# Kernel tuning notes

Measured on AMD Instinct MI355X. Metric: run time of the kernel, lower is better.

The kernel has to match this reference:

```python
import jax, jax.numpy as jnp
import numpy as np

N_NODES = 100000
N_EDGES = 1600000
IN_CH = 128
OUT_CH = 128
N_REL = 8


def setup_inputs() -> dict:
    key = jax.random.key(0)
    k1, k2, k3, k4, k5, k6 = jax.random.split(key, 6)
    x = jax.random.normal(k1, (N_NODES, IN_CH), dtype=jnp.float32)
    edge_index = jax.random.randint(k2, (2, N_EDGES), 0, N_NODES, dtype=jnp.int64)
    edge_type = jax.random.randint(k3, (N_EDGES,), 0, N_REL, dtype=jnp.int64)
    # learned parameters (PyG RGCNConv: per-relation weight, root weight, bias)
    scale = 1.0 / np.sqrt(IN_CH)
    weight = jax.random.normal(k4, (N_REL, IN_CH, OUT_CH), dtype=jnp.float32) * scale
    root = jax.random.normal(k5, (IN_CH, OUT_CH), dtype=jnp.float32) * scale
    bias = jax.random.normal(k6, (OUT_CH,), dtype=jnp.float32) * 0.01
    return {"x": x, "edge_index": edge_index, "edge_type": edge_type,
            "weight": weight, "root": root, "bias": bias}


def reference(x, edge_index, edge_type, weight, root, bias):
    # PyG RGCNConv forward: out_i = x_i @ root + bias
    #   + sum_r mean_{j in N_r(i)} (x_j @ W_r)   (default aggr='mean' per relation)
    N = x.shape[0]
    R, _, O = weight.shape
    src, dst = edge_index[0], edge_index[1]
    # transform all nodes under every relation once: [R, N, O]
    xW = jnp.einsum('ni,rio->rno', x, weight)
    msg = xW[edge_type, src]                      # [E, O] per-edge message
    seg = edge_type * N + dst                     # segment per (relation, dst)
    sums = jax.ops.segment_sum(msg, seg, num_segments=R * N)        # [R*N, O]
    cnt = jax.ops.segment_sum(jnp.ones_like(msg[:, 0]), seg, num_segments=R * N)
    mean = sums / jnp.maximum(cnt, 1.0)[:, None]
    agg = mean.reshape(R, N, O).sum(axis=0)       # sum over relations
    return agg + x @ root + bias
```

## Files before the change

kernel.cpp:

```cpp
#include <hip/hip_runtime.h>
#include <hip/hip_bf16.h>
#include <stdint.h>

#define N_NODES 100000
#define N_EDGES 1600000
#define CH 128
#define N_REL 8
#define N_PAD 100096
#define N_KEYS (N_NODES * N_REL)

#define NBKT 782
#define NSUB 64
#define SUBCAP 128
#define BKT_STRIDE (NSUB * SUBCAP)
#define CUR_PAD 16
#define N_KEYS_PAD (NBKT * 1024)

using frag_ab = __attribute__((ext_vector_type(8))) short;
using frag_cd = __attribute__((ext_vector_type(4))) float;

__device__ __forceinline__ short f2bs(float f) {
    union { __hip_bfloat16 h; short s; } u;
    u.h = __float2bfloat16(f);
    return u.s;
}

__device__ __forceinline__ uint32_t pack2bf(float a, float b) {
    union { __hip_bfloat16 h; unsigned short s; } ua, ub;
    ua.h = __float2bfloat16(a); ub.h = __float2bfloat16(b);
    return (uint32_t)ua.s | ((uint32_t)ub.s << 16);
}

__device__ __forceinline__ float bf_lo(uint32_t u) { return __uint_as_float(u << 16); }
__device__ __forceinline__ float bf_hi(uint32_t u) { return __uint_as_float(u & 0xffff0000u); }


__global__ __launch_bounds__(256)
void prep_kernel(const int* __restrict__ ei, const int* __restrict__ et,
                 int* __restrict__ cur, uint32_t* __restrict__ bucket,
                 const float* __restrict__ x, short* __restrict__ xb,
                 const float* __restrict__ root, const float* __restrict__ W,
                 short* __restrict__ Bsw) {
    const int tid = threadIdx.x;
    const int g = blockIdx.x * 256 + tid;

    if (g < N_EDGES) {
        int dst = ei[N_EDGES + g];
        int src = ei[g];
        int r = et[g];
        int b = dst >> 7;
        int sub = blockIdx.x & (NSUB - 1);
        int pos = atomicAdd(&cur[(sub * NBKT + b) * CUR_PAD], 1);
        if (pos < SUBCAP)
            bucket[((size_t)b * NSUB + sub) * SUBCAP + pos] =
                ((uint32_t)src << 10) | ((uint32_t)(dst & 127) << 3) | (uint32_t)r;
    }

    if (g < N_NODES * CH / 8) {
        const float4* xp = (const float4*)x;
        float4 a = xp[(size_t)g * 2], bb = xp[(size_t)g * 2 + 1];
        frag_ab f;
        f[0] = f2bs(a.x); f[1] = f2bs(a.y); f[2] = f2bs(a.z); f[3] = f2bs(a.w);
        f[4] = f2bs(bb.x); f[5] = f2bs(bb.y); f[6] = f2bs(bb.z); f[7] = f2bs(bb.w);
        *(frag_ab*)(xb + (size_t)g * 8) = f;
    }

    if (g < 9 * 2048) {
        int chunk = g >> 11, entry = g & 2047;
        int m16 = entry & 15, ct = (entry >> 4) & 7, quad = (entry >> 7) & 3, ks = entry >> 9;
        const float* src = (chunk == 0) ? root : W + (size_t)(chunk - 1) * CH * CH;
        int col = ct * 16 + m16, kb = ks * 32 + quad * 8;
        frag_ab f;
#pragma unroll
        for (int j = 0; j < 8; ++j) f[j] = f2bs(src[(size_t)(kb + j) * CH + col]);
        *(frag_ab*)(Bsw + (size_t)g * 8) = f;
    }
}

__global__ __launch_bounds__(512)
void bin_kernel(const int* __restrict__ cur, const uint32_t* __restrict__ bucket,
                int* __restrict__ perm, int* __restrict__ ends) {
    __shared__ int hist[1024];
    __shared__ int cursor[1024];
    __shared__ int sh[512];
    __shared__ int lens[NSUB];
    const int tid = threadIdx.x;
    const int b = blockIdx.x;
    const size_t bbase = (size_t)b * BKT_STRIDE;
    hist[tid] = 0; hist[tid + 512] = 0;
    if (tid < NSUB) {
        int n = cur[(tid * NBKT + b) * CUR_PAD];
        lens[tid] = (n > SUBCAP) ? SUBCAP : n;
    }
    __syncthreads();
    for (int j = tid; j < BKT_STRIDE; j += 512) {
        const int sub = j >> 7;
        const int i = j & (SUBCAP - 1);
        if (i < lens[sub])
            atomicAdd(&hist[bucket[bbase + j] & 1023], 1);
    }
    __syncthreads();
    const int a0 = hist[2 * tid], a1 = hist[2 * tid + 1];
    const int s2 = a0 + a1;
    sh[tid] = s2;
    __syncthreads();
    for (int st = 1; st < 512; st <<= 1) {
        int u = (tid >= st) ? sh[tid - st] : 0;
        __syncthreads();
        sh[tid] += u;
        __syncthreads();
    }
    const int excl = sh[tid] - s2;
    cursor[2 * tid]     = excl;
    cursor[2 * tid + 1] = excl + a0;
    ends[b * 1024 + 2 * tid]     = (int)bbase + excl + a0;
    ends[b * 1024 + 2 * tid + 1] = (int)bbase + excl + a0 + a1;
    __syncthreads();
    for (int j = tid; j < BKT_STRIDE; j += 512) {
        const int sub = j >> 7;
        const int i = j & (SUBCAP - 1);
        if (i < lens[sub]) {
            const uint32_t e = bucket[bbase + j];
            const int pos = atomicAdd(&cursor[e & 1023], 1);
            perm[bbase + pos] = (int)(e >> 10);
        }
    }
}

#define ACC16(U0, U1)                                           \
    do {                                                        \
        a0 += bf_lo((U0).x);  a1 += bf_hi((U0).x);              \
        a2 += bf_lo((U0).y);  a3 += bf_hi((U0).y);              \
        a4 += bf_lo((U0).z);  a5 += bf_hi((U0).z);              \
        a6 += bf_lo((U0).w);  a7 += bf_hi((U0).w);              \
        a8 += bf_lo((U1).x);  a9 += bf_hi((U1).x);              \
        a10 += bf_lo((U1).y); a11 += bf_hi((U1).y);             \
        a12 += bf_lo((U1).z); a13 += bf_hi((U1).z);             \
        a14 += bf_lo((U1).w); a15 += bf_hi((U1).w);             \
    } while (0)

__global__ __launch_bounds__(512, 4)
void rgcn_fused(const int* __restrict__ ends, const int* __restrict__ perm,
                const short* __restrict__ xb, const short* __restrict__ Bsw,
                const float* __restrict__ bias, float* __restrict__ out) {
    __shared__ short Ash[128 * 128];
    __shared__ int lends[1026];
    const int tid = threadIdx.x;
    const int wave = tid >> 6, lane = tid & 63;
    const int m16 = lane & 15, quad = lane >> 4;
    const int grp = lane >> 3, sub = lane & 7;
    const int wm = wave >> 2, wn = wave & 3;
    const long B0 = (long)blockIdx.x * 128;

    for (int i = tid; i < 1025; i += 512)
        lends[i] = (i == 0) ? (int)(blockIdx.x * BKT_STRIDE)
                            : ends[(size_t)blockIdx.x * 1024 + i - 1];

    float bcol[2];
#pragma unroll
    for (int ct = 0; ct < 2; ++ct) bcol[ct] = bias[wn * 32 + ct * 16 + m16];

    frag_cd acc[4][2];
#pragma unroll
    for (int mt = 0; mt < 4; ++mt)
#pragma unroll
        for (int ct = 0; ct < 2; ++ct) acc[mt][ct] = (frag_cd){0.f, 0.f, 0.f, 0.f};

    __syncthreads();

#pragma unroll
    for (int ks = 0; ks < 4; ++ks) {
        frag_ab af[4];
#pragma unroll
        for (int mt = 0; mt < 4; ++mt)
            af[mt] = *(const frag_ab*)(xb + (B0 + wm * 64 + mt * 16 + m16) * CH + ks * 32 + quad * 8);
#pragma unroll
        for (int ct = 0; ct < 2; ++ct) {
            frag_ab bf = *(const frag_ab*)(Bsw + (size_t)((((ks * 4 + quad) * 8) + wn * 2 + ct) * 16 + m16) * 8);
#pragma unroll
            for (int mt = 0; mt < 4; ++mt)
                acc[mt][ct] = __builtin_amdgcn_mfma_f32_16x16x32_bf16(af[mt], bf, acc[mt][ct], 0, 0, 0);
        }
    }

    const uint32_t ch32 = (uint32_t)sub << 5;
    const char* xbp = (const char*)xb;

    for (int r = 0; r < N_REL; ++r) {
#pragma unroll
        for (int step = 0; step < 2; ++step) {
            const int lrow = (wave << 4) + (step << 3) + grp;
            const int keyL = lrow * 8 + r;
            const int s = lends[keyL];
            const int e = lends[keyL + 1];
            float a0 = 0.f, a1 = 0.f, a2 = 0.f, a3 = 0.f;
            float a4 = 0.f, a5 = 0.f, a6 = 0.f, a7 = 0.f;
            float a8 = 0.f, a9 = 0.f, a10 = 0.f, a11 = 0.f;
            float a12 = 0.f, a13 = 0.f, a14 = 0.f, a15 = 0.f;
            int p0 = perm[(s < e) ? s : 0];
            int p1 = perm[(s + 1 < e) ? s + 1 : ((s < e) ? s : 0)];
            for (int k = s; k < e; k += 2) {
                const char* b0 = xbp + (((size_t)(uint32_t)p0 << 8) | ch32);
                const char* b1 = xbp + (((size_t)(uint32_t)p1 << 8) | ch32);
                const uint4 u0 = *(const uint4*)(b0);
                const uint4 u1 = *(const uint4*)(b0 + 16);
                const uint4 u2 = *(const uint4*)(b1);
                const uint4 u3 = *(const uint4*)(b1 + 16);
                const int kn = k + 2;
                p0 = perm[(kn < e) ? kn : 0];
                p1 = perm[(kn + 1 < e) ? kn + 1 : 0];
                ACC16(u0, u1);
                if (k + 1 < e) ACC16(u2, u3);
            }
            const int c = e - s;
            const float sc = (c > 1) ? (1.0f / (float)c) : 1.0f;
            uint4 w0, w1;
            w0.x = pack2bf(a0 * sc, a1 * sc);
            w0.y = pack2bf(a2 * sc, a3 * sc);
            w0.z = pack2bf(a4 * sc, a5 * sc);
            w0.w = pack2bf(a6 * sc, a7 * sc);
            w1.x = pack2bf(a8 * sc, a9 * sc);
            w1.y = pack2bf(a10 * sc, a11 * sc);
            w1.z = pack2bf(a12 * sc, a13 * sc);
            w1.w = pack2bf(a14 * sc, a15 * sc);
            char* drow = (char*)Ash + lrow * 256;
            const int swz = lrow & 7;
            *(uint4*)(drow + ((((sub << 1)    ) ^ swz) << 4)) = w0;
            *(uint4*)(drow + ((((sub << 1) | 1) ^ swz) << 4)) = w1;
        }
        __syncthreads();
        const short* Bc = Bsw + (size_t)(r + 1) * 2048 * 8;
#pragma unroll
        for (int ks = 0; ks < 4; ++ks) {
            frag_ab af[4];
#pragma unroll
            for (int mt = 0; mt < 4; ++mt) {
                const int lr = wm * 64 + mt * 16 + m16;
                af[mt] = *(const frag_ab*)((const char*)Ash + lr * 256 + (((ks * 4 + quad) ^ (lr & 7)) << 4));
            }
#pragma unroll
            for (int ct = 0; ct < 2; ++ct) {
                frag_ab bf = *(const frag_ab*)(Bc + (size_t)((((ks * 4 + quad) * 8) + wn * 2 + ct) * 16 + m16) * 8);
#pragma unroll
                for (int mt = 0; mt < 4; ++mt)
                    acc[mt][ct] = __builtin_amdgcn_mfma_f32_16x16x32_bf16(af[mt], bf, acc[mt][ct], 0, 0, 0);
            }
        }
        __syncthreads();
    }

#pragma unroll
    for (int mt = 0; mt < 4; ++mt) {
#pragma unroll
        for (int ct = 0; ct < 2; ++ct) {
            const long row0 = B0 + wm * 64 + mt * 16 + quad * 4;
            const int col = wn * 32 + ct * 16 + m16;
#pragma unroll
            for (int rg = 0; rg < 4; ++rg) {
                const long rr = row0 + rg;
                if (rr < N_NODES) out[rr * CH + col] = acc[mt][ct][rg] + bcol[ct];
            }
        }
    }
}


__global__ void count_rd_kernel(const int* __restrict__ ei, const int* __restrict__ et,
                                int* __restrict__ cnt) {
    int e = blockIdx.x * 256 + threadIdx.x;
    if (e < N_EDGES) {
        int dst = ei[N_EDGES + e];
        int r = et[e];
        atomicAdd(&cnt[r * N_NODES + dst], 1);
    }
}

__global__ void scatter_kernel(const int* __restrict__ ei, const int* __restrict__ et,
                               const float* __restrict__ x, float* __restrict__ sums,
                               int rel) {
    int gid = (blockIdx.x * 256 + threadIdx.x) >> 5;
    int lane = threadIdx.x & 31;
    int ngroups = gridDim.x * 8;
    for (int e = gid; e < N_EDGES; e += ngroups) {
        if (et[e] != rel) continue;
        int src = ei[e];
        int dst = ei[N_EDGES + e];
        float4 v = ((const float4*)(x + (size_t)src * CH))[lane];
        float* s = sums + (size_t)dst * CH + (size_t)lane * 4;
        atomicAdd(s + 0, v.x);
        atomicAdd(s + 1, v.y);
        atomicAdd(s + 2, v.z);
        atomicAdd(s + 3, v.w);
    }
}

__global__ __launch_bounds__(256, 2)
void gemm_kernel(const float* __restrict__ A, const float* __restrict__ B,
                 const float* __restrict__ bias, const int* __restrict__ cnt,
                 float* __restrict__ out, int accumulate) {
    const int wave = threadIdx.x >> 6;
    const int lane = threadIdx.x & 63;
    const int m16 = lane & 15;
    const int quad = lane >> 4;

    frag_ab bfrag[4][8];
#pragma unroll
    for (int ks = 0; ks < 4; ++ks) {
        const int kb = ks * 32 + quad * 8;
#pragma unroll
        for (int ct = 0; ct < 8; ++ct) {
            const int col = ct * 16 + m16;
            frag_ab f;
#pragma unroll
            for (int j = 0; j < 8; ++j)
                f[j] = f2bs(B[(size_t)(kb + j) * CH + col]);
            bfrag[ks][ct] = f;
        }
    }

    const int nstrips = (N_NODES + 63) / 64;
    for (int strip = blockIdx.x; strip < nstrips; strip += gridDim.x) {
        const int row = strip * 64 + wave * 16 + m16;
        const bool valid = row < N_NODES;
        float scale = 1.0f;
        if (cnt != nullptr && valid) {
            int c = cnt[row];
            if (c > 1) scale = 1.0f / (float)c;
        }
        const float4* arow = (const float4*)(A + (size_t)(valid ? row : 0) * CH);
        frag_cd acc[8];
#pragma unroll
        for (int ct = 0; ct < 8; ++ct) acc[ct] = (frag_cd){0.f, 0.f, 0.f, 0.f};
#pragma unroll
        for (int ks = 0; ks < 4; ++ks) {
            float4 a0 = arow[ks * 8 + quad * 2];
            float4 a1 = arow[ks * 8 + quad * 2 + 1];
            frag_ab af;
            af[0] = f2bs(a0.x * scale); af[1] = f2bs(a0.y * scale);
            af[2] = f2bs(a0.z * scale); af[3] = f2bs(a0.w * scale);
            af[4] = f2bs(a1.x * scale); af[5] = f2bs(a1.y * scale);
            af[6] = f2bs(a1.z * scale); af[7] = f2bs(a1.w * scale);
#pragma unroll
            for (int ct = 0; ct < 8; ++ct)
                acc[ct] = __builtin_amdgcn_mfma_f32_16x16x32_bf16(af, bfrag[ks][ct], acc[ct], 0, 0, 0);
        }
        const int obase = strip * 64 + wave * 16 + quad * 4;
#pragma unroll
        for (int ct = 0; ct < 8; ++ct) {
            const int col = ct * 16 + m16;
#pragma unroll
            for (int rg = 0; rg < 4; ++rg) {
                const int r = obase + rg;
                if (r < N_NODES) {
                    const size_t idx = (size_t)r * CH + col;
                    if (accumulate) out[idx] += acc[ct][rg];
                    else out[idx] = acc[ct][rg] + bias[col];
                }
            }
        }
    }
}

__global__ void edge_transform_kernel(const int* __restrict__ ei, const int* __restrict__ et,
                                      const float* __restrict__ x, const float* __restrict__ W,
                                      const int* __restrict__ cnt, float* __restrict__ out) {
    __shared__ float xs[CH];
    const int tid = threadIdx.x;
    for (int e = blockIdx.x; e < N_EDGES; e += gridDim.x) {
        const int src = ei[e];
        const int dst = ei[N_EDGES + e];
        const int r = et[e];
        __syncthreads();
        xs[tid] = x[(size_t)src * CH + tid];
        __syncthreads();
        const int c = cnt[r * N_NODES + dst];
        const float scale = (c > 1) ? (1.0f / (float)c) : 1.0f;
        const float* Wr = W + (size_t)r * CH * CH;
        float acc = 0.f;
#pragma unroll 8
        for (int k = 0; k < CH; ++k) acc += xs[k] * Wr[(size_t)k * CH + tid];
        atomicAdd(&out[(size_t)dst * CH + tid], acc * scale);
    }
}


static inline size_t al512(size_t x) { return (x + 511) & ~(size_t)511; }

extern "C" void kernel_launch(void* const* d_in, const int* in_sizes, int n_in,
                              void* d_out, int out_size, void* d_ws, size_t ws_size,
                              hipStream_t stream) {
    const float* x    = (const float*)d_in[0];
    const int*   ei   = (const int*)d_in[1];
    const int*   et   = (const int*)d_in[2];
    const float* W    = (const float*)d_in[3];
    const float* root = (const float*)d_in[4];
    const float* bias = (const float*)d_in[5];
    float* out = (float*)d_out;

    size_t o = 0;
    const size_t o_cur  = o; o += al512((size_t)NSUB * NBKT * CUR_PAD * 4);
    const size_t o_bkt  = o; o += al512((size_t)NBKT * BKT_STRIDE * 4);
    const size_t o_perm = o; o += al512((size_t)NBKT * BKT_STRIDE * 4);
    const size_t o_ends = o; o += al512((size_t)N_KEYS_PAD * 4);
    const size_t o_bsw  = o; o += al512((size_t)9 * 2048 * 16);
    const size_t o_xb   = o; o += al512((size_t)N_PAD * CH * 2);
    const size_t need_t1 = o;

    const size_t cnt_bytes = (size_t)N_REL * N_NODES * sizeof(int);
    const size_t cnt_rsv   = al512(cnt_bytes);
    const size_t sums51    = (size_t)N_NODES * CH * sizeof(float);

    char* ws = (char*)d_ws;
    if (ws_size >= need_t1) {
        int*      cur    = (int*)(ws + o_cur);
        uint32_t* bucket = (uint32_t*)(ws + o_bkt);
        int*      perm   = (int*)(ws + o_perm);
        int*      endsA  = (int*)(ws + o_ends);
        short*    Bsw    = (short*)(ws + o_bsw);
        short*    xb     = (short*)(ws + o_xb);

        hipMemsetAsync(cur, 0, (size_t)NSUB * NBKT * CUR_PAD * 4, stream);
        prep_kernel<<<(N_EDGES + 255) / 256, 256, 0, stream>>>(
            ei, et, cur, bucket, x, xb, root, W, Bsw);
        bin_kernel<<<NBKT, 512, 0, stream>>>(cur, bucket, perm, endsA);
        rgcn_fused<<<NBKT, 512, 0, stream>>>(endsA, perm, xb, Bsw, bias, out);
    } else if (ws_size >= cnt_rsv + sums51) {
        int*   cnt  = (int*)d_ws;
        float* sums = (float*)((char*)d_ws + cnt_rsv);
        hipMemsetAsync(cnt, 0, cnt_bytes, stream);
        count_rd_kernel<<<(N_EDGES + 255) / 256, 256, 0, stream>>>(ei, et, cnt);
        gemm_kernel<<<512, 256, 0, stream>>>(x, root, bias, nullptr, out, 0);
        for (int r = 0; r < N_REL; ++r) {
            hipMemsetAsync(sums, 0, sums51, stream);
            scatter_kernel<<<6400, 256, 0, stream>>>(ei, et, x, sums, r);
            gemm_kernel<<<512, 256, 0, stream>>>(sums, W + (size_t)r * CH * CH,
                                                 nullptr, cnt + (size_t)r * N_NODES, out, 1);
        }
    } else {
        int* cnt = (int*)d_ws;
        hipMemsetAsync(cnt, 0, cnt_bytes, stream);
        count_rd_kernel<<<(N_EDGES + 255) / 256, 256, 0, stream>>>(ei, et, cnt);
        gemm_kernel<<<512, 256, 0, stream>>>(x, root, bias, nullptr, out, 0);
        edge_transform_kernel<<<65536, CH, 0, stream>>>(ei, et, x, W, cnt, out);
    }
}
```

Measured before the change: 327.5 us.

## Fuse bucket binning into aggregation kernel with LDS-resident permutation

Merges bin_kernel into the main RGCN kernel so each block sorts its own bucket in shared memory and keeps the permutation in LDS, spilling to global only past a capacity. This removes one kernel launch and the global round trips for perm and ends. It also changes the gather mapping to four threads per row, each handling 64 channels with 32 accumulators instead of 8 threads with 16. The extra LDS (16KB for perm) and higher register pressure may reduce occupancy.

```diff
diff --git a/kernel.cpp b/kernel.cpp
--- a/kernel.cpp
+++ b/kernel.cpp
@@ -14,7 +14,7 @@
 #define SUBCAP 128
 #define BKT_STRIDE (NSUB * SUBCAP)
 #define CUR_PAD 16
-#define N_KEYS_PAD (NBKT * 1024)
+#define PERM_LDS_CAP 4096
 
 using frag_ab = __attribute__((ext_vector_type(8))) short;
 using frag_cd = __attribute__((ext_vector_type(4))) float;
@@ -77,84 +77,73 @@
     }
 }
 
-__global__ __launch_bounds__(512)
-void bin_kernel(const int* __restrict__ cur, const uint32_t* __restrict__ bucket,
-                int* __restrict__ perm, int* __restrict__ ends) {
-    __shared__ int hist[1024];
-    __shared__ int cursor[1024];
-    __shared__ int sh[512];
+#define ACC_U4(U, B)                                            \
+    do {                                                        \
+        a[(B)+0] += bf_lo((U).x); a[(B)+1] += bf_hi((U).x);     \
+        a[(B)+2] += bf_lo((U).y); a[(B)+3] += bf_hi((U).y);     \
+        a[(B)+4] += bf_lo((U).z); a[(B)+5] += bf_hi((U).z);     \
+        a[(B)+6] += bf_lo((U).w); a[(B)+7] += bf_hi((U).w);     \
+    } while (0)
+
+__global__ __launch_bounds__(512, 4)
+void rgcn_mega(const int* __restrict__ cur, const uint32_t* __restrict__ bucket,
+               int* __restrict__ perm_spill,
+               const short* __restrict__ xb, const short* __restrict__ Bsw,
+               const float* __restrict__ bias, float* __restrict__ out) {
+    __shared__ short Ash[128 * 128];
+    __shared__ int perm_lds[PERM_LDS_CAP];
+    __shared__ int lends[1025];
     __shared__ int lens[NSUB];
+    int* hist   = (int*)Ash;
+    int* cursor = (int*)Ash + 1024;
+    int* shl    = (int*)Ash + 2048;
+
     const int tid = threadIdx.x;
+    const int wave = tid >> 6, lane = tid & 63;
+    const int m16 = lane & 15, quad = lane >> 4;
+    const int wm = wave >> 2, wn = wave & 3;
     const int b = blockIdx.x;
     const size_t bbase = (size_t)b * BKT_STRIDE;
+    const long B0 = (long)b * 128;
+
+#define PERM(idx) (((idx) < PERM_LDS_CAP) ? perm_lds[(idx)] : perm_spill[bbase + (idx)])
+
     hist[tid] = 0; hist[tid + 512] = 0;
+    if (tid == 0) perm_lds[0] = 0;
     if (tid < NSUB) {
         int n = cur[(tid * NBKT + b) * CUR_PAD];
         lens[tid] = (n > SUBCAP) ? SUBCAP : n;
     }
     __syncthreads();
-    for (int j = tid; j < BKT_STRIDE; j += 512) {
-        const int sub = j >> 7;
-        const int i = j & (SUBCAP - 1);
-        if (i < lens[sub])
+    for (int j = tid; j < BKT_STRIDE; j += 512)
+        if ((j & (SUBCAP - 1)) < lens[j >> 7])
             atomicAdd(&hist[bucket[bbase + j] & 1023], 1);
-    }
     __syncthreads();
-    const int a0 = hist[2 * tid], a1 = hist[2 * tid + 1];
-    const int s2 = a0 + a1;
-    sh[tid] = s2;
+    const int h0 = hist[2 * tid], h1 = hist[2 * tid + 1];
+    const int s2 = h0 + h1;
+    shl[tid] = s2;
     __syncthreads();
     for (int st = 1; st < 512; st <<= 1) {
-        int u = (tid >= st) ? sh[tid - st] : 0;
-        __syncthreads();
-        sh[tid] += u;
-        __syncthreads();
-    }
-    const int excl = sh[tid] - s2;
+        int u = (tid >= st) ? shl[tid - st] : 0;
+        __syncthreads();
+        shl[tid] += u;
+        __syncthreads();
+    }
+    const int excl = shl[tid] - s2;
     cursor[2 * tid]     = excl;
-    cursor[2 * tid + 1] = excl + a0;
-    ends[b * 1024 + 2 * tid]     = (int)bbase + excl + a0;
-    ends[b * 1024 + 2 * tid + 1] = (int)bbase + excl + a0 + a1;
+    cursor[2 * tid + 1] = excl + h0;
+    if (tid == 0) lends[0] = 0;
+    lends[1 + 2 * tid] = excl + h0;
+    lends[2 + 2 * tid] = excl + h0 + h1;
     __syncthreads();
-    for (int j = tid; j < BKT_STRIDE; j += 512) {
-        const int sub = j >> 7;
-        const int i = j & (SUBCAP - 1);
-        if (i < lens[sub]) {
+    for (int j = tid; j < BKT_STRIDE; j += 512)
+        if ((j & (SUBCAP - 1)) < lens[j >> 7]) {
             const uint32_t e = bucket[bbase + j];
             const int pos = atomicAdd(&cursor[e & 1023], 1);
-            perm[bbase + pos] = (int)(e >> 10);
-        }
-    }
-}
-
-#define ACC16(U0, U1)                                           \
-    do {                                                        \
-        a0 += bf_lo((U0).x);  a1 += bf_hi((U0).x);              \
-        a2 += bf_lo((U0).y);  a3 += bf_hi((U0).y);              \
-        a4 += bf_lo((U0).z);  a5 += bf_hi((U0).z);              \
-        a6 += bf_lo((U0).w);  a7 += bf_hi((U0).w);              \
-        a8 += bf_lo((U1).x);  a9 += bf_hi((U1).x);              \
-        a10 += bf_lo((U1).y); a11 += bf_hi((U1).y);             \
-        a12 += bf_lo((U1).z); a13 += bf_hi((U1).z);             \
-        a14 += bf_lo((U1).w); a15 += bf_hi((U1).w);             \
-    } while (0)
-
-__global__ __launch_bounds__(512, 4)
-void rgcn_fused(const int* __restrict__ ends, const int* __restrict__ perm,
-                const short* __restrict__ xb, const short* __restrict__ Bsw,
-                const float* __restrict__ bias, float* __restrict__ out) {
-    __shared__ short Ash[128 * 128];
-    __shared__ int lends[1026];
-    const int tid = threadIdx.x;
-    const int wave = tid >> 6, lane = tid & 63;
-    const int m16 = lane & 15, quad = lane >> 4;
-    const int grp = lane >> 3, sub = lane & 7;
-    const int wm = wave >> 2, wn = wave & 3;
-    const long B0 = (long)blockIdx.x * 128;
-
-    for (int i = tid; i < 1025; i += 512)
-        lends[i] = (i == 0) ? (int)(blockIdx.x * BKT_STRIDE)
-                            : ends[(size_t)blockIdx.x * 1024 + i - 1];
+            const int v = (int)(e >> 10);
+            if (pos < PERM_LDS_CAP) perm_lds[pos] = v;
+            else perm_spill[bbase + pos] = v;
+        }
 
     float bcol[2];
 #pragma unroll
@@ -165,8 +154,6 @@
     for (int mt = 0; mt < 4; ++mt)
 #pragma unroll
         for (int ct = 0; ct < 2; ++ct) acc[mt][ct] = (frag_cd){0.f, 0.f, 0.f, 0.f};
-
-    __syncthreads();
 
 #pragma unroll
     for (int ks = 0; ks < 4; ++ks) {
@@ -182,51 +169,52 @@
                 acc[mt][ct] = __builtin_amdgcn_mfma_f32_16x16x32_bf16(af[mt], bf, acc[mt][ct], 0, 0, 0);
         }
     }
-
-    const uint32_t ch32 = (uint32_t)sub << 5;
+    __syncthreads();
+
+    const int lrow = tid >> 2;
+    const int q4 = tid & 3;
+    const uint32_t ch64 = (uint32_t)q4 << 6;
     const char* xbp = (const char*)xb;
+    char* drow = (char*)Ash + lrow * 256;
+    const int swz = lrow & 7;
 
     for (int r = 0; r < N_REL; ++r) {
-#pragma unroll
-        for (int step = 0; step < 2; ++step) {
-            const int lrow = (wave << 4) + (step << 3) + grp;
-            const int keyL = lrow * 8 + r;
-            const int s = lends[keyL];
-            const int e = lends[keyL + 1];
-            float a0 = 0.f, a1 = 0.f, a2 = 0.f, a3 = 0.f;
-            float a4 = 0.f, a5 = 0.f, a6 = 0.f, a7 = 0.f;
-            float a8 = 0.f, a9 = 0.f, a10 = 0.f, a11 = 0.f;
-            float a12 = 0.f, a13 = 0.f, a14 = 0.f, a15 = 0.f;
-            int p0 = perm[(s < e) ? s : 0];
-            int p1 = perm[(s + 1 < e) ? s + 1 : ((s < e) ? s : 0)];
-            for (int k = s; k < e; k += 2) {
-                const char* b0 = xbp + (((size_t)(uint32_t)p0 << 8) | ch32);
-                const char* b1 = xbp + (((size_t)(uint32_t)p1 << 8) | ch32);
-                const uint4 u0 = *(const uint4*)(b0);
-                const uint4 u1 = *(const uint4*)(b0 + 16);
-                const uint4 u2 = *(const uint4*)(b1);
-                const uint4 u3 = *(const uint4*)(b1 + 16);
-                const int kn = k + 2;
-                p0 = perm[(kn < e) ? kn : 0];
-                p1 = perm[(kn + 1 < e) ? kn + 1 : 0];
-                ACC16(u0, u1);
-                if (k + 1 < e) ACC16(u2, u3);
-            }
-            const int c = e - s;
-            const float sc = (c > 1) ? (1.0f / (float)c) : 1.0f;
-            uint4 w0, w1;
-            w0.x = pack2bf(a0 * sc, a1 * sc);
-            w0.y = pack2bf(a2 * sc, a3 * sc);
-            w0.z = pack2bf(a4 * sc, a5 * sc);
-            w0.w = pack2bf(a6 * sc, a7 * sc);
-            w1.x = pack2bf(a8 * sc, a9 * sc);
-            w1.y = pack2bf(a10 * sc, a11 * sc);
-            w1.z = pack2bf(a12 * sc, a13 * sc);
-            w1.w = pack2bf(a14 * sc, a15 * sc);
-            char* drow = (char*)Ash + lrow * 256;
-            const int swz = lrow & 7;
-            *(uint4*)(drow + ((((sub << 1)    ) ^ swz) << 4)) = w0;
-            *(uint4*)(drow + ((((sub << 1) | 1) ^ swz) << 4)) = w1;
+        const int keyL = lrow * 8 + r;
+        const int s = lends[keyL];
+        const int e = lends[keyL + 1];
+        float a[32];
+#pragma unroll
+        for (int i = 0; i < 32; ++i) a[i] = 0.f;
+        int p0 = PERM((s < e) ? s : 0);
+        int p1 = PERM((s + 1 < e) ? s + 1 : ((s < e) ? s : 0));
+        for (int k = s; k < e; k += 2) {
+            const char* c0 = xbp + (((size_t)(uint32_t)p0 << 8) | ch64);
+            const char* c1 = xbp + (((size_t)(uint32_t)p1 << 8) | ch64);
+            const uint4 u0 = *(const uint4*)(c0);
+            const uint4 u1 = *(const uint4*)(c0 + 16);
+            const uint4 u2 = *(const uint4*)(c0 + 32);
+            const uint4 u3 = *(const uint4*)(c0 + 48);
+            const uint4 u4 = *(const uint4*)(c1);
+            const uint4 u5 = *(const uint4*)(c1 + 16);
+            const uint4 u6 = *(const uint4*)(c1 + 32);
+            const uint4 u7 = *(const uint4*)(c1 + 48);
+            const bool two = (k + 1 < e);
+            const int kn = k + 2;
+            p0 = PERM((kn < e) ? kn : 0);
+            p1 = PERM((kn + 1 < e) ? kn + 1 : 0);
+            ACC_U4(u0, 0); ACC_U4(u1, 8); ACC_U4(u2, 16); ACC_U4(u3, 24);
+            if (two) { ACC_U4(u4, 0); ACC_U4(u5, 8); ACC_U4(u6, 16); ACC_U4(u7, 24); }
+        }
+        const int c = e - s;
+        const float sc = (c > 1) ? (1.0f / (float)c) : 1.0f;
+#pragma unroll
+        for (int t = 0; t < 4; ++t) {
+            uint4 w;
+            w.x = pack2bf(a[t * 8 + 0] * sc, a[t * 8 + 1] * sc);
+            w.y = pack2bf(a[t * 8 + 2] * sc, a[t * 8 + 3] * sc);
+            w.z = pack2bf(a[t * 8 + 4] * sc, a[t * 8 + 5] * sc);
+            w.w = pack2bf(a[t * 8 + 6] * sc, a[t * 8 + 7] * sc);
+            *(uint4*)(drow + (((q4 * 4 + t) ^ swz) << 4)) = w;
         }
         __syncthreads();
         const short* Bc = Bsw + (size_t)(r + 1) * 2048 * 8;
@@ -248,6 +236,7 @@
         }
         __syncthreads();
     }
+#undef PERM
 
 #pragma unroll
     for (int mt = 0; mt < 4; ++mt) {
@@ -401,7 +390,6 @@
     const size_t o_cur  = o; o += al512((size_t)NSUB * NBKT * CUR_PAD * 4);
     const size_t o_bkt  = o; o += al512((size_t)NBKT * BKT_STRIDE * 4);
     const size_t o_perm = o; o += al512((size_t)NBKT * BKT_STRIDE * 4);
-    const size_t o_ends = o; o += al512((size_t)N_KEYS_PAD * 4);
     const size_t o_bsw  = o; o += al512((size_t)9 * 2048 * 16);
     const size_t o_xb   = o; o += al512((size_t)N_PAD * CH * 2);
     const size_t need_t1 = o;
@@ -415,15 +403,13 @@
         int*      cur    = (int*)(ws + o_cur);
         uint32_t* bucket = (uint32_t*)(ws + o_bkt);
         int*      perm   = (int*)(ws + o_perm);
-        int*      endsA  = (int*)(ws + o_ends);
         short*    Bsw    = (short*)(ws + o_bsw);
         short*    xb     = (short*)(ws + o_xb);
 
         hipMemsetAsync(cur, 0, (size_t)NSUB * NBKT * CUR_PAD * 4, stream);
         prep_kernel<<<(N_EDGES + 255) / 256, 256, 0, stream>>>(
             ei, et, cur, bucket, x, xb, root, W, Bsw);
-        bin_kernel<<<NBKT, 512, 0, stream>>>(cur, bucket, perm, endsA);
-        rgcn_fused<<<NBKT, 512, 0, stream>>>(endsA, perm, xb, Bsw, bias, out);
+        rgcn_mega<<<NBKT, 512, 0, stream>>>(cur, bucket, perm, xb, Bsw, bias, out);
     } else if (ws_size >= cnt_rsv + sums51) {
         int*   cnt  = (int*)d_ws;
         float* sums = (float*)((char*)d_ws + cnt_rsv);
```

Result: no change. 325.9 us (-0.5%).
